# Kernel optimization log

Measured on AMD Instinct MI355X. Metric: run time of the kernel, lower is better.

The kernel has to match this reference:

```python
import jax, jax.numpy as jnp
import numpy as np

H = 256      # hidden_dim
NH = 8       # num_heads
D = H // NH  # per-head dim
NEG = -(2.0**32) + 1.0
EPS = 1e-5


def setup_inputs() -> dict:
    key = jax.random.key(0)
    ks = jax.random.split(key, 12)
    N, Tq, Tk = 2, 2048, 2048
    s = 1.0 / np.sqrt(H)
    return {
        "Q": jax.random.normal(ks[0], (N, Tq, H), jnp.float32),
        "K": jax.random.normal(ks[1], (N, Tk, H), jnp.float32),
        "V": jax.random.normal(ks[2], (N, Tk, H), jnp.float32),
        "Wq": jax.random.normal(ks[3], (H, H), jnp.float32) * s,
        "bq": jnp.zeros((H,), jnp.float32),
        "Wk": jax.random.normal(ks[4], (H, H), jnp.float32) * s,
        "bk": jnp.zeros((H,), jnp.float32),
        "Wv": jax.random.normal(ks[5], (H, H), jnp.float32) * s,
        "bv": jnp.zeros((H,), jnp.float32),
        "gamma": jnp.ones((H,), jnp.float32),
        "beta": jnp.zeros((H,), jnp.float32),
    }


def _split_heads(x):
    # [N,T,H] -> [h,N,T,D]  (matches torch split(dim=2)+cat(dim=0): head-major)
    N, T, _ = x.shape
    return x.reshape(N, T, NH, D).transpose(2, 0, 1, 3)


def reference(Q, K, V, Wq, bq, Wk, bk, Wv, bv, gamma, beta):
    N, Tq, _ = Q.shape
    Tk = K.shape[1]
    Ql = jax.nn.relu(Q @ Wq + bq)
    Kl = jax.nn.relu(K @ Wk + bk)
    Vl = jax.nn.relu(V @ Wv + bv)
    Qh, Kh, Vh = _split_heads(Ql), _split_heads(Kl), _split_heads(Vl)

    scores = jnp.einsum("hnqd,hnkd->hnqk", Qh, Kh) / jnp.sqrt(jnp.float32(D))
    key_mask = jnp.sign(jnp.abs(K).sum(-1))    # [N,Tk]
    scores = jnp.where(key_mask[None, :, None, :] == 0, NEG, scores)
    attn = jax.nn.softmax(scores / 0.01, axis=-1)
    query_mask = jnp.sign(jnp.abs(Q).sum(-1))  # [N,Tq]
    attn = attn * query_mask[None, :, :, None]  # dropout p=0 -> identity

    ctx = jnp.einsum("hnqk,hnkd->hnqd", attn[..., :-1], Vh[:, :, :-1, :])
    out = ctx.transpose(1, 2, 0, 3).reshape(N, Tq, H)

    mu = out.mean(-1, keepdims=True)
    var = ((out - mu) ** 2).mean(-1, keepdims=True)
    out = (out - mu) / jnp.sqrt(var + EPS) * gamma + beta

    weight = attn.transpose(1, 2, 0, 3).reshape(N, Tq, NH * Tk).mean(-1)
    return out, weight
```

## Files before the change

### kernel.cpp

```cpp
#include <hip/hip_runtime.h>
#include <math.h>

#define H_DIM 256
#define NHEAD 8
#define DHEAD 32
#define NB 2
#define TSEQ 2048
#define LN_EPS 1e-5f

#define QK2_SCALE 25.503486f
#define SPLIT 4
#define TILES_PER (TSEQ / 64 / SPLIT)

typedef _Float16 half8 __attribute__((ext_vector_type(8)));
typedef _Float16 half2t __attribute__((ext_vector_type(2)));
typedef float f32x4 __attribute__((ext_vector_type(4)));

__device__ __forceinline__ f32x4 mfma16(half8 a, half8 b, f32x4 c) {
  return __builtin_amdgcn_mfma_f32_16x16x32_f16(a, b, c, 0, 0, 0);
}
__device__ __forceinline__ float exp2fast(float x) {
  return __builtin_amdgcn_exp2f(x);
}
__device__ __forceinline__ half2t pkrtz(float a, float b) {
  return __builtin_bit_cast(half2t, __builtin_amdgcn_cvt_pkrtz(a, b));
}

__global__ __launch_bounds__(256) void mask_kernel(
    const float* __restrict__ Q, const float* __restrict__ K,
    float* __restrict__ qmask, float* __restrict__ kmask) {
  const int wid = threadIdx.x >> 6, lane = threadIdx.x & 63;
  int row = blockIdx.x * 4 + wid;
  const int total_q = NB * TSEQ;
  const float* src;
  float* dst;
  if (row < total_q) { src = Q + (size_t)row * H_DIM; dst = qmask + row; }
  else               { src = K + (size_t)(row - total_q) * H_DIM; dst = kmask + (row - total_q); }
  float4 v = *(const float4*)(src + lane * 4);
  float s = fabsf(v.x) + fabsf(v.y) + fabsf(v.z) + fabsf(v.w);
  #pragma unroll
  for (int off = 32; off > 0; off >>= 1) s += __shfl_xor(s, off);
  if (lane == 0) *dst = (s != 0.0f) ? 1.0f : 0.0f;
}

__global__ __launch_bounds__(256) void prepack_kernel(
    const float* __restrict__ Wq, const float* __restrict__ Wk, const float* __restrict__ Wv,
    half8* __restrict__ WpkHi, half8* __restrict__ WpkLo) {
  int slot = blockIdx.x * 256 + threadIdx.x;
  int lane = slot & 63;
  int fg = (slot >> 6) & 15;
  int s  = (slot >> 10) & 7;
  int which = slot >> 13;
  const float* W = which == 0 ? Wq : which == 1 ? Wk : Wv;
  int j  = fg * 16 + (lane & 15);
  int kb = s * 32 + (lane >> 4) * 8;
  half8 hi, lo;
  #pragma unroll
  for (int jj = 0; jj < 8; ++jj) {
    float x = W[(size_t)(kb + jj) * H_DIM + j];
    _Float16 h = (_Float16)x;
    hi[jj] = h;
    lo[jj] = (_Float16)(x - (float)h);
  }
  WpkHi[slot] = hi;
  WpkLo[slot] = lo;
}

__global__ __launch_bounds__(256) void proj_kernel(
    const float* __restrict__ Q, const float* __restrict__ K, const float* __restrict__ V,
    const float* __restrict__ bq, const float* __restrict__ bk, const float* __restrict__ bv,
    const half8* __restrict__ WpkHi, const half8* __restrict__ WpkLo,
    float* __restrict__ Qh, float* __restrict__ Kh, float* __restrict__ Vh) {
  const int which = blockIdx.z;
  const float* X    = which == 0 ? Q  : which == 1 ? K  : V;
  const float* bias = which == 0 ? bq : which == 1 ? bk : bv;
  float* dst        = which == 0 ? Qh : which == 1 ? Kh : Vh;

  const int tid = threadIdx.x;
  const int w = tid >> 6, lane = tid & 63;
  const int l15 = lane & 15, quad = lane >> 4;
  const int mbase = blockIdx.y * 64;
  const int nfg   = blockIdx.x * 4;

  half8 ahi[8], alo[8];
  {
    const float* xrow = X + (size_t)(mbase + w * 16 + l15) * H_DIM + quad * 8;
    #pragma unroll
    for (int s = 0; s < 8; ++s) {
      float4 a0 = *(const float4*)(xrow + s * 32);
      float4 a1 = *(const float4*)(xrow + s * 32 + 4);
      float xs[8] = {a0.x, a0.y, a0.z, a0.w, a1.x, a1.y, a1.z, a1.w};
      #pragma unroll
      for (int i = 0; i < 8; ++i) {
        _Float16 h = (_Float16)xs[i];
        ahi[s][i] = h;
        alo[s][i] = (_Float16)(xs[i] - (float)h);
      }
    }
  }

  f32x4 acc[4];
  #pragma unroll
  for (int f = 0; f < 4; ++f) acc[f] = (f32x4){0.f, 0.f, 0.f, 0.f};

  #pragma unroll
  for (int s = 0; s < 8; ++s) {
    const half8* ph = WpkHi + (((size_t)which * 8 + s) * 16 + nfg) * 64 + lane;
    const half8* pl = WpkLo + (((size_t)which * 8 + s) * 16 + nfg) * 64 + lane;
    #pragma unroll
    for (int f = 0; f < 4; ++f) {
      half8 BH = ph[f * 64];
      half8 BL = pl[f * 64];
      acc[f] = mfma16(ahi[s], BH, acc[f]);
      acc[f] = mfma16(ahi[s], BL, acc[f]);
      acc[f] = mfma16(alo[s], BH, acc[f]);
    }
  }

  #pragma unroll
  for (int f = 0; f < 4; ++f) {
    int j = blockIdx.x * 64 + f * 16 + l15;
    float bj = bias[j];
    int hh = j >> 5, dd = j & 31;
    #pragma unroll
    for (int r = 0; r < 4; ++r) {
      int m = mbase + w * 16 + quad * 4 + r;
      int n = m >> 11, t = m & (TSEQ - 1);
      float val = fmaxf(acc[f][r] + bj, 0.0f);
      if (which == 2 && t == TSEQ - 1) val = 0.0f;
      dst[(((size_t)hh * NB + n) * TSEQ + t) * DHEAD + dd] = val;
    }
  }
}

__global__ __launch_bounds__(256) void repack_kernel(
    const float* __restrict__ Qh, const float* __restrict__ Kh, const float* __restrict__ Vh,
    const float* __restrict__ kmask,
    half8* __restrict__ Gqhi, half8* __restrict__ Gqlo,
    half8* __restrict__ Gkhi, half8* __restrict__ Gklo, half8* __restrict__ Gv,
    half8* __restrict__ AmaskF) {
  const int tile = blockIdx.x;
  const int hn   = blockIdx.y;
  const int which = blockIdx.z;
  const int tid = threadIdx.x;
  if (which < 2) {
    const int w = tid >> 6, lane = tid & 63;
    const int f = w, krlo = lane & 15, kdc = lane >> 4;
    const float* src = (which == 0 ? Qh : Kh) +
        ((size_t)hn * TSEQ + tile * 64 + f * 16 + krlo) * DHEAD + kdc * 8;
    float4 a0 = *(const float4*)src;
    float4 a1 = *(const float4*)(src + 4);
    float xs[8] = {a0.x, a0.y, a0.z, a0.w, a1.x, a1.y, a1.z, a1.w};
    const float sc = which == 0 ? QK2_SCALE : 1.0f;
    half8 hi, lo;
    #pragma unroll
    for (int i = 0; i < 8; ++i) {
      float x = xs[i] * sc;
      _Float16 h = (_Float16)x;
      hi[i] = h;
      lo[i] = (_Float16)(x - (float)h);
    }
    size_t di = ((size_t)hn * 32 + tile) * 256 + f * 64 + kdc * 16 + krlo;
    if (which == 0) { Gqhi[di] = hi; Gqlo[di] = lo; }
    else            { Gkhi[di] = hi; Gklo[di] = lo; }
  } else if (which == 2) {
    const int s = tid;
    const int top = s >> 6, mid = (s >> 4) & 3, low = s & 15;
    const int c = top >> 1, hh = top & 1;
    const int vkg = c * 4 + mid, vd = hh * 16 + low;
    const int n = hn & 1;
    const float* src = Vh + ((size_t)hn * TSEQ + tile * 64 + vkg * 8) * DHEAD + vd;
    const float* kmp = kmask + (size_t)n * TSEQ + tile * 64 + vkg * 8;
    half8 v8;
    #pragma unroll
    for (int j = 0; j < 8; ++j) v8[j] = (_Float16)(src[j * DHEAD] * kmp[j]);
    Gv[((size_t)hn * 32 + tile) * 256 + s] = v8;
  } else {
    if (hn >= NB || tid >= 128) return;
    const int n = hn;
    const int c = tid >> 6, lane = tid & 63;
    const int quad = lane >> 4, l15 = lane & 15;
    half8 am;
    #pragma unroll
    for (int j = 0; j < 8; ++j)
      am[j] = (l15 == 0) ? (_Float16)kmask[(size_t)n * TSEQ + tile * 64 + c * 32 + quad * 8 + j]
                         : (_Float16)0.0f;
    AmaskF[(((size_t)n * 32 + tile) * 2 + c) * 64 + lane] = am;
  }
}

__global__ __launch_bounds__(256) void attn_kernel(
    const half8* __restrict__ Gqhi, const half8* __restrict__ Gqlo,
    const half8* __restrict__ Gkhi, const half8* __restrict__ Gklo,
    const half8* __restrict__ Gv, const half8* __restrict__ AmaskF,
    float* __restrict__ Op, float* __restrict__ Mp, float* __restrict__ Lp) {
  __shared__ __align__(16) half8 Vf[2][256];
  __shared__ __align__(16) _Float16 Pbuf[4][16][72];

  const int tid = threadIdx.x;
  const int w = tid >> 6, lane = tid & 63;
  const int l15 = lane & 15, quad = lane >> 4;

  const int b = blockIdx.x;
  const int g    = ((b & 7) << 1) | ((b >> 3) & 1);
  const int qt   = (b >> 4) & 31;
  const int sblk = b >> 9;
  const int n = g & 1;

  const size_t fbase = (size_t)g * 32 * 256;
  const int tile0 = sblk * TILES_PER;

  half8 qhi = Gqhi[fbase + (size_t)qt * 256 + w * 64 + lane];
  half8 qlo = Gqlo[fbase + (size_t)qt * 256 + w * 64 + lane];

  float m_q = -1.0e30f;
  f32x4 O0, O1, Ol;
  O0 = (f32x4){0.f, 0.f, 0.f, 0.f};
  O1 = (f32x4){0.f, 0.f, 0.f, 0.f};
  Ol = (f32x4){0.f, 0.f, 0.f, 0.f};

  const half8* kh  = Gkhi + fbase + (size_t)tile0 * 256 + lane;
  const half8* kl  = Gklo + fbase + (size_t)tile0 * 256 + lane;
  const half8* gv  = Gv   + fbase + (size_t)tile0 * 256 + tid;
  const half8* amp = AmaskF + (((size_t)n * 32 + tile0) * 2) * 64 + lane;

  half8 KH[4], KL[4];
  #pragma unroll
  for (int f = 0; f < 4; ++f) { KH[f] = kh[f * 64]; KL[f] = kl[f * 64]; }
  Vf[0][tid] = gv[0];

  #pragma unroll
  for (int tt = 0; tt < TILES_PER; ++tt) {
    half8 KHn[4], KLn[4], vnext;
    if (tt < TILES_PER - 1) {
      #pragma unroll
      for (int f = 0; f < 4; ++f) { KHn[f] = kh[256 + f * 64]; KLn[f] = kl[256 + f * 64]; }
      vnext = gv[256];
    }
    half8 am0 = amp[0];
    half8 am1 = amp[64];

    __syncthreads();
    if (tt < TILES_PER - 1)
      Vf[(tt + 1) & 1][tid] = vnext;

    f32x4 S[4];
    #pragma unroll
    for (int f = 0; f < 4; ++f) {
      f32x4 a = (f32x4){0.f, 0.f, 0.f, 0.f};
      a = mfma16(KL[f], qhi, a);
      a = mfma16(KH[f], qlo, a);
      a = mfma16(KH[f], qhi, a);
      S[f] = a;
    }

    float t0 = fmaxf(fmaxf(S[0][0], S[0][1]), fmaxf(S[0][2], S[0][3]));
    float t1 = fmaxf(fmaxf(S[1][0], S[1][1]), fmaxf(S[1][2], S[1][3]));
    float t2 = fmaxf(fmaxf(S[2][0], S[2][1]), fmaxf(S[2][2], S[2][3]));
    float t3 = fmaxf(fmaxf(S[3][0], S[3][1]), fmaxf(S[3][2], S[3][3]));
    float mx = fmaxf(fmaxf(t0, t1), fmaxf(t2, t3));
    mx = fmaxf(mx, __shfl_xor(mx, 16));
    mx = fmaxf(mx, __shfl_xor(mx, 32));

    float mnew = fmaxf(m_q, mx);
    float alpha = exp2fast(m_q - mnew);
    m_q = mnew;

    #pragma unroll
    for (int f = 0; f < 4; ++f) {
      float p0 = exp2fast(S[f][0] - m_q);
      float p1 = exp2fast(S[f][1] - m_q);
      float p2 = exp2fast(S[f][2] - m_q);
      float p3 = exp2fast(S[f][3] - m_q);
      half2t a01 = pkrtz(p0, p1);
      half2t a23 = pkrtz(p2, p3);
      *(half2t*)&Pbuf[w][l15][f * 16 + quad * 4]     = a01;
      *(half2t*)&Pbuf[w][l15][f * 16 + quad * 4 + 2] = a23;
    }
    #pragma unroll
    for (int r = 0; r < 4; ++r) { O0[r] *= alpha; O1[r] *= alpha; }
    Ol[0] *= alpha;
    asm volatile("s_waitcnt lgkmcnt(0)" ::: "memory");

    const half8* vbuf = (const half8*)Vf[tt & 1];
    #pragma unroll
    for (int c = 0; c < 2; ++c) {
      half8 pb = *(const half8*)&Pbuf[w][l15][c * 32 + quad * 8];
      O0 = mfma16(vbuf[(c * 2 + 0) * 64 + lane], pb, O0);
      O1 = mfma16(vbuf[(c * 2 + 1) * 64 + lane], pb, O1);
      Ol = mfma16(c == 0 ? am0 : am1, pb, Ol);
    }

    #pragma unroll
    for (int f = 0; f < 4; ++f) { KH[f] = KHn[f]; KL[f] = KLn[f]; }
    kh += 256; kl += 256; gv += 256; amp += 128;
  }

  {
    int q = qt * 64 + w * 16 + l15;
    size_t idx = ((size_t)(sblk * 16 + g) * TSEQ + q) * DHEAD;
    *(f32x4*)&Op[idx + quad * 4]      = O0;
    *(f32x4*)&Op[idx + 16 + quad * 4] = O1;
    if (quad == 0) {
      Mp[(size_t)(sblk * 16 + g) * TSEQ + q] = m_q;
      Lp[(size_t)(sblk * 16 + g) * TSEQ + q] = Ol[0];
    }
  }
}

__global__ __launch_bounds__(256) void ln_kernel(
    const float* __restrict__ Op, const float* __restrict__ Mp, const float* __restrict__ Lp,
    const float* __restrict__ gamma, const float* __restrict__ beta,
    const float* __restrict__ qmask,
    float* __restrict__ out, float* __restrict__ wout) {
  const int wid = threadIdx.x >> 6, lane = threadIdx.x & 63;
  const int row = blockIdx.x * 4 + wid;
  const int n = row >> 11, q = row & (TSEQ - 1);
  const int hh = lane >> 3;
  const int hn = hh * NB + n;
  const int dbase = (lane & 7) * 4;

  float4 P[SPLIT];
  float m[SPLIT], l[SPLIT];
  #pragma unroll
  for (int i = 0; i < SPLIT; ++i) {
    size_t si = (size_t)(i * 16 + hn) * TSEQ + q;
    P[i] = *(const float4*)(Op + si * DHEAD + dbase);
    m[i] = Mp[si];
    l[i] = Lp[si];
  }
  float mm = fmaxf(fmaxf(m[0], m[1]), fmaxf(m[2], m[3]));
  float denom = 0.f;
  float a[SPLIT];
  #pragma unroll
  for (int i = 0; i < SPLIT; ++i) { a[i] = exp2fast(m[i] - mm); denom += l[i] * a[i]; }
  float qm = qmask[row];
  float inv = qm / denom;

  float4 x = make_float4(0.f, 0.f, 0.f, 0.f);
  #pragma unroll
  for (int i = 0; i < SPLIT; ++i) {
    x.x += P[i].x * a[i]; x.y += P[i].y * a[i];
    x.z += P[i].z * a[i]; x.w += P[i].w * a[i];
  }
  x.x *= inv; x.y *= inv; x.z *= inv; x.w *= inv;

  float s = x.x + x.y + x.z + x.w;
  #pragma unroll
  for (int off = 32; off > 0; off >>= 1) s += __shfl_xor(s, off);
  float mu = s * (1.0f / H_DIM);
  float dx0 = x.x - mu, dx1 = x.y - mu, dx2 = x.z - mu, dx3 = x.w - mu;
  float sq = dx0 * dx0 + dx1 * dx1 + dx2 * dx2 + dx3 * dx3;
  #pragma unroll
  for (int off = 32; off > 0; off >>= 1) sq += __shfl_xor(sq, off);
  float rstd = rsqrtf(sq * (1.0f / H_DIM) + LN_EPS);
  float4 g = *(const float4*)(gamma + lane * 4);
  float4 bb = *(const float4*)(beta + lane * 4);
  float4 y;
  y.x = dx0 * rstd * g.x + bb.x;
  y.y = dx1 * rstd * g.y + bb.y;
  y.z = dx2 * rstd * g.z + bb.z;
  y.w = dx3 * rstd * g.w + bb.w;
  *(float4*)(out + (size_t)row * H_DIM + lane * 4) = y;
  if (lane == 0) wout[row] = qm * (1.0f / TSEQ);
}

extern "C" void kernel_launch(void* const* d_in, const int* in_sizes, int n_in,
                              void* d_out, int out_size, void* d_ws, size_t ws_size,
                              hipStream_t stream) {
  const float* Q  = (const float*)d_in[0];
  const float* K  = (const float*)d_in[1];
  const float* V  = (const float*)d_in[2];
  const float* Wq = (const float*)d_in[3];
  const float* bq = (const float*)d_in[4];
  const float* Wk = (const float*)d_in[5];
  const float* bk = (const float*)d_in[6];
  const float* Wv = (const float*)d_in[7];
  const float* bv = (const float*)d_in[8];
  const float* gamma = (const float*)d_in[9];
  const float* beta  = (const float*)d_in[10];

  float* ws = (float*)d_ws;
  const size_t perHN = (size_t)16 * TSEQ * DHEAD;
  float* Qh = ws;
  float* Kh = Qh + perHN;
  float* Vh = Kh + perHN;
  float* Opart = ws;
  float* tail = ws + 4 * perHN;
  const size_t NFRAG = (size_t)16 * 32 * 256;
  half8* Gqhi = (half8*)tail;
  half8* Gqlo = Gqhi + NFRAG;
  half8* Gkhi = Gqlo + NFRAG;
  half8* Gklo = Gkhi + NFRAG;
  half8* Gv   = Gklo + NFRAG;
  float* Mp = (float*)(Gv + NFRAG);
  float* Lp = Mp + SPLIT * 16 * TSEQ;
  float* qmask = Lp + SPLIT * 16 * TSEQ;
  float* kmask = qmask + NB * TSEQ;
  half8* WpkHi = (half8*)(kmask + NB * TSEQ);
  half8* WpkLo = WpkHi + 24576;
  half8* AmaskF = WpkLo + 24576;

  float* out  = (float*)d_out;
  float* wout = out + (size_t)NB * TSEQ * H_DIM;

  hipLaunchKernelGGL(mask_kernel, dim3(2 * NB * TSEQ / 4), dim3(256), 0, stream,
                     Q, K, qmask, kmask);
  hipLaunchKernelGGL(prepack_kernel, dim3(96), dim3(256), 0, stream,
                     Wq, Wk, Wv, WpkHi, WpkLo);
  hipLaunchKernelGGL(proj_kernel, dim3(H_DIM / 64, NB * TSEQ / 64, 3), dim3(256), 0, stream,
                     Q, K, V, bq, bk, bv, WpkHi, WpkLo, Qh, Kh, Vh);
  hipLaunchKernelGGL(repack_kernel, dim3(32, 16, 4), dim3(256), 0, stream,
                     Qh, Kh, Vh, kmask, Gqhi, Gqlo, Gkhi, Gklo, Gv, AmaskF);
  hipLaunchKernelGGL(attn_kernel, dim3(16 * 32 * SPLIT), dim3(256), 0, stream,
                     Gqhi, Gqlo, Gkhi, Gklo, Gv, AmaskF, Opart, Mp, Lp);
  hipLaunchKernelGGL(ln_kernel, dim3(NB * TSEQ / 4), dim3(256), 0, stream,
                     Opart, Mp, Lp, gamma, beta, qmask, out, wout);
}
```

Before: 143.3 us.

## Fuse repack into projection via LDS transpose and store attention partials as fp16

```diff
diff --git a/kernel.cpp b/kernel.cpp
--- a/kernel.cpp
+++ b/kernel.cpp
@@ -13,6 +13,7 @@
 #define TILES_PER (TSEQ / 64 / SPLIT)
 
 typedef _Float16 half8 __attribute__((ext_vector_type(8)));
+typedef _Float16 half4t __attribute__((ext_vector_type(4)));
 typedef _Float16 half2t __attribute__((ext_vector_type(2)));
 typedef float f32x4 __attribute__((ext_vector_type(4)));
 
@@ -45,7 +46,24 @@
 
 __global__ __launch_bounds__(256) void prepack_kernel(
     const float* __restrict__ Wq, const float* __restrict__ Wk, const float* __restrict__ Wv,
-    half8* __restrict__ WpkHi, half8* __restrict__ WpkLo) {
+    const float* __restrict__ kmask,
+    half8* __restrict__ WpkHi, half8* __restrict__ WpkLo, half8* __restrict__ AmaskF) {
+  if (blockIdx.x >= 96) {
+    int slot2 = (blockIdx.x - 96) * 256 + threadIdx.x;
+    int n = slot2 >> 12;
+    int rem = slot2 & 4095;
+    int tile = rem >> 7;
+    int c = (rem >> 6) & 1;
+    int lane = rem & 63;
+    int quad = lane >> 4, l15 = lane & 15;
+    half8 am;
+    #pragma unroll
+    for (int j = 0; j < 8; ++j)
+      am[j] = (l15 == 0) ? (_Float16)kmask[(size_t)n * TSEQ + tile * 64 + c * 32 + quad * 8 + j]
+                         : (_Float16)0.0f;
+    AmaskF[(((size_t)n * 32 + tile) * 2 + c) * 64 + lane] = am;
+    return;
+  }
   int slot = blockIdx.x * 256 + threadIdx.x;
   int lane = slot & 63;
   int fg = (slot >> 6) & 15;
@@ -70,17 +88,22 @@
     const float* __restrict__ Q, const float* __restrict__ K, const float* __restrict__ V,
     const float* __restrict__ bq, const float* __restrict__ bk, const float* __restrict__ bv,
     const half8* __restrict__ WpkHi, const half8* __restrict__ WpkLo,
-    float* __restrict__ Qh, float* __restrict__ Kh, float* __restrict__ Vh) {
+    const float* __restrict__ kmask,
+    half8* __restrict__ Gqhi, half8* __restrict__ Gqlo,
+    half8* __restrict__ Gkhi, half8* __restrict__ Gklo, half8* __restrict__ Gv) {
   const int which = blockIdx.z;
   const float* X    = which == 0 ? Q  : which == 1 ? K  : V;
   const float* bias = which == 0 ? bq : which == 1 ? bk : bv;
-  float* dst        = which == 0 ? Qh : which == 1 ? Kh : Vh;
+
+  __shared__ __align__(16) float T[64 * 68];
 
   const int tid = threadIdx.x;
   const int w = tid >> 6, lane = tid & 63;
   const int l15 = lane & 15, quad = lane >> 4;
   const int mbase = blockIdx.y * 64;
   const int nfg   = blockIdx.x * 4;
+  const int nn   = mbase >> 11;
+  const int tile = blockIdx.y & 31;
 
   half8 ahi[8], alo[8];
   {
@@ -119,73 +142,59 @@
 
   #pragma unroll
   for (int f = 0; f < 4; ++f) {
-    int j = blockIdx.x * 64 + f * 16 + l15;
-    float bj = bias[j];
-    int hh = j >> 5, dd = j & 31;
+    float bj = bias[blockIdx.x * 64 + f * 16 + l15];
     #pragma unroll
     for (int r = 0; r < 4; ++r) {
-      int m = mbase + w * 16 + quad * 4 + r;
-      int n = m >> 11, t = m & (TSEQ - 1);
+      int row = w * 16 + quad * 4 + r;
       float val = fmaxf(acc[f][r] + bj, 0.0f);
-      if (which == 2 && t == TSEQ - 1) val = 0.0f;
-      dst[(((size_t)hh * NB + n) * TSEQ + t) * DHEAD + dd] = val;
-    }
-  }
-}
-
-__global__ __launch_bounds__(256) void repack_kernel(
-    const float* __restrict__ Qh, const float* __restrict__ Kh, const float* __restrict__ Vh,
-    const float* __restrict__ kmask,
-    half8* __restrict__ Gqhi, half8* __restrict__ Gqlo,
-    half8* __restrict__ Gkhi, half8* __restrict__ Gklo, half8* __restrict__ Gv,
-    half8* __restrict__ AmaskF) {
-  const int tile = blockIdx.x;
-  const int hn   = blockIdx.y;
-  const int which = blockIdx.z;
-  const int tid = threadIdx.x;
+      if (which == 2 && ((mbase + row) & (TSEQ - 1)) == TSEQ - 1) val = 0.0f;
+      T[row * 68 + f * 16 + l15] = val;
+    }
+  }
+  __syncthreads();
+
   if (which < 2) {
-    const int w = tid >> 6, lane = tid & 63;
-    const int f = w, krlo = lane & 15, kdc = lane >> 4;
-    const float* src = (which == 0 ? Qh : Kh) +
-        ((size_t)hn * TSEQ + tile * 64 + f * 16 + krlo) * DHEAD + kdc * 8;
-    float4 a0 = *(const float4*)src;
-    float4 a1 = *(const float4*)(src + 4);
-    float xs[8] = {a0.x, a0.y, a0.z, a0.w, a1.x, a1.y, a1.z, a1.w};
-    const float sc = which == 0 ? QK2_SCALE : 1.0f;
-    half8 hi, lo;
-    #pragma unroll
-    for (int i = 0; i < 8; ++i) {
-      float x = xs[i] * sc;
-      _Float16 h = (_Float16)x;
-      hi[i] = h;
-      lo[i] = (_Float16)(x - (float)h);
-    }
-    size_t di = ((size_t)hn * 32 + tile) * 256 + f * 64 + kdc * 16 + krlo;
-    if (which == 0) { Gqhi[di] = hi; Gqlo[di] = lo; }
-    else            { Gkhi[di] = hi; Gklo[di] = lo; }
-  } else if (which == 2) {
-    const int s = tid;
-    const int top = s >> 6, mid = (s >> 4) & 3, low = s & 15;
+    const int fq = tid >> 6, lp = tid & 63;
+    const int kdc = lp >> 4, krlo = lp & 15;
+    const int row = fq * 16 + krlo;
+    const float sc = (which == 0) ? QK2_SCALE : 1.0f;
+    #pragma unroll
+    for (int hs = 0; hs < 2; ++hs) {
+      const float* p = &T[row * 68 + hs * 32 + kdc * 8];
+      float4 a0 = *(const float4*)p;
+      float4 a1 = *(const float4*)(p + 4);
+      float xs[8] = {a0.x, a0.y, a0.z, a0.w, a1.x, a1.y, a1.z, a1.w};
+      half8 hi, lo;
+      #pragma unroll
+      for (int i = 0; i < 8; ++i) {
+        float x = xs[i] * sc;
+        _Float16 h = (_Float16)x;
+        hi[i] = h;
+        lo[i] = (_Float16)(x - (float)h);
+      }
+      int hn = (blockIdx.x * 2 + hs) * NB + nn;
+      size_t di = ((size_t)hn * 32 + tile) * 256 + tid;
+      if (which == 0) { Gqhi[di] = hi; Gqlo[di] = lo; }
+      else            { Gkhi[di] = hi; Gklo[di] = lo; }
+    }
+  } else {
+    const int top = tid >> 6, mid = (tid >> 4) & 3, low = tid & 15;
     const int c = top >> 1, hh = top & 1;
-    const int vkg = c * 4 + mid, vd = hh * 16 + low;
-    const int n = hn & 1;
-    const float* src = Vh + ((size_t)hn * TSEQ + tile * 64 + vkg * 8) * DHEAD + vd;
-    const float* kmp = kmask + (size_t)n * TSEQ + tile * 64 + vkg * 8;
-    half8 v8;
-    #pragma unroll
-    for (int j = 0; j < 8; ++j) v8[j] = (_Float16)(src[j * DHEAD] * kmp[j]);
-    Gv[((size_t)hn * 32 + tile) * 256 + s] = v8;
-  } else {
-    if (hn >= NB || tid >= 128) return;
-    const int n = hn;
-    const int c = tid >> 6, lane = tid & 63;
-    const int quad = lane >> 4, l15 = lane & 15;
-    half8 am;
+    const int trow0 = (c * 4 + mid) * 8;
+    float km[8];
     #pragma unroll
     for (int j = 0; j < 8; ++j)
-      am[j] = (l15 == 0) ? (_Float16)kmask[(size_t)n * TSEQ + tile * 64 + c * 32 + quad * 8 + j]
-                         : (_Float16)0.0f;
-    AmaskF[(((size_t)n * 32 + tile) * 2 + c) * 64 + lane] = am;
+      km[j] = kmask[(size_t)nn * TSEQ + tile * 64 + trow0 + j];
+    #pragma unroll
+    for (int hs = 0; hs < 2; ++hs) {
+      const int col = hs * 32 + hh * 16 + low;
+      half8 v8;
+      #pragma unroll
+      for (int j = 0; j < 8; ++j)
+        v8[j] = (_Float16)(T[(trow0 + j) * 68 + col] * km[j]);
+      int hn = (blockIdx.x * 2 + hs) * NB + nn;
+      Gv[((size_t)hn * 32 + tile) * 256 + tid] = v8;
+    }
   }
 }
 
@@ -193,7 +202,7 @@
     const half8* __restrict__ Gqhi, const half8* __restrict__ Gqlo,
     const half8* __restrict__ Gkhi, const half8* __restrict__ Gklo,
     const half8* __restrict__ Gv, const half8* __restrict__ AmaskF,
-    float* __restrict__ Op, float* __restrict__ Mp, float* __restrict__ Lp) {
+    _Float16* __restrict__ Opf, float* __restrict__ Mp, float* __restrict__ Lp) {
   __shared__ __align__(16) half8 Vf[2][256];
   __shared__ __align__(16) _Float16 Pbuf[4][16][72];
 
@@ -299,8 +308,10 @@
   {
     int q = qt * 64 + w * 16 + l15;
     size_t idx = ((size_t)(sblk * 16 + g) * TSEQ + q) * DHEAD;
-    *(f32x4*)&Op[idx + quad * 4]      = O0;
-    *(f32x4*)&Op[idx + 16 + quad * 4] = O1;
+    half4t o0 = {(_Float16)O0[0], (_Float16)O0[1], (_Float16)O0[2], (_Float16)O0[3]};
+    half4t o1 = {(_Float16)O1[0], (_Float16)O1[1], (_Float16)O1[2], (_Float16)O1[3]};
+    *(half4t*)&Opf[idx + quad * 4]      = o0;
+    *(half4t*)&Opf[idx + 16 + quad * 4] = o1;
     if (quad == 0) {
       Mp[(size_t)(sblk * 16 + g) * TSEQ + q] = m_q;
       Lp[(size_t)(sblk * 16 + g) * TSEQ + q] = Ol[0];
@@ -309,7 +320,7 @@
 }
 
 __global__ __launch_bounds__(256) void ln_kernel(
-    const float* __restrict__ Op, const float* __restrict__ Mp, const float* __restrict__ Lp,
+    const _Float16* __restrict__ Opf, const float* __restrict__ Mp, const float* __restrict__ Lp,
     const float* __restrict__ gamma, const float* __restrict__ beta,
     const float* __restrict__ qmask,
     float* __restrict__ out, float* __restrict__ wout) {
@@ -320,12 +331,12 @@
   const int hn = hh * NB + n;
   const int dbase = (lane & 7) * 4;
 
-  float4 P[SPLIT];
   float m[SPLIT], l[SPLIT];
+  half4t P[SPLIT];
   #pragma unroll
   for (int i = 0; i < SPLIT; ++i) {
     size_t si = (size_t)(i * 16 + hn) * TSEQ + q;
-    P[i] = *(const float4*)(Op + si * DHEAD + dbase);
+    P[i] = *(const half4t*)&Opf[si * DHEAD + dbase];
     m[i] = Mp[si];
     l[i] = Lp[si];
   }
@@ -340,8 +351,8 @@
   float4 x = make_float4(0.f, 0.f, 0.f, 0.f);
   #pragma unroll
   for (int i = 0; i < SPLIT; ++i) {
-    x.x += P[i].x * a[i]; x.y += P[i].y * a[i];
-    x.z += P[i].z * a[i]; x.w += P[i].w * a[i];
+    x.x += (float)P[i][0] * a[i]; x.y += (float)P[i][1] * a[i];
+    x.z += (float)P[i][2] * a[i]; x.w += (float)P[i][3] * a[i];
   }
   x.x *= inv; x.y *= inv; x.z *= inv; x.w *= inv;
 
@@ -380,15 +391,10 @@
   const float* gamma = (const float*)d_in[9];
   const float* beta  = (const float*)d_in[10];
 
-  float* ws = (float*)d_ws;
-  const size_t perHN = (size_t)16 * TSEQ * DHEAD;
-  float* Qh = ws;
-  float* Kh = Qh + perHN;
-  float* Vh = Kh + perHN;
-  float* Opart = ws;
-  float* tail = ws + 4 * perHN;
+  char* ws = (char*)d_ws;
   const size_t NFRAG = (size_t)16 * 32 * 256;
-  half8* Gqhi = (half8*)tail;
+  _Float16* Opf = (_Float16*)ws;
+  half8* Gqhi = (half8*)(ws + (size_t)SPLIT * 16 * TSEQ * DHEAD * 2);
   half8* Gqlo = Gqhi + NFRAG;
   half8* Gkhi = Gqlo + NFRAG;
   half8* Gklo = Gkhi + NFRAG;
@@ -406,14 +412,13 @@
 
   hipLaunchKernelGGL(mask_kernel, dim3(2 * NB * TSEQ / 4), dim3(256), 0, stream,
                      Q, K, qmask, kmask);
-  hipLaunchKernelGGL(prepack_kernel, dim3(96), dim3(256), 0, stream,
-                     Wq, Wk, Wv, WpkHi, WpkLo);
+  hipLaunchKernelGGL(prepack_kernel, dim3(128), dim3(256), 0, stream,
+                     Wq, Wk, Wv, kmask, WpkHi, WpkLo, AmaskF);
   hipLaunchKernelGGL(proj_kernel, dim3(H_DIM / 64, NB * TSEQ / 64, 3), dim3(256), 0, stream,
-                     Q, K, V, bq, bk, bv, WpkHi, WpkLo, Qh, Kh, Vh);
-  hipLaunchKernelGGL(repack_kernel, dim3(32, 16, 4), dim3(256), 0, stream,
-                     Qh, Kh, Vh, kmask, Gqhi, Gqlo, Gkhi, Gklo, Gv, AmaskF);
+                     Q, K, V, bq, bk, bv, WpkHi, WpkLo, kmask,
+                     Gqhi, Gqlo, Gkhi, Gklo, Gv);
   hipLaunchKernelGGL(attn_kernel, dim3(16 * 32 * SPLIT), dim3(256), 0, stream,
-                     Gqhi, Gqlo, Gkhi, Gklo, Gv, AmaskF, Opart, Mp, Lp);
+                     Gqhi, Gqlo, Gkhi, Gklo, Gv, AmaskF, Opf, Mp, Lp);
   hipLaunchKernelGGL(ln_kernel, dim3(NB * TSEQ / 4), dim3(256), 0, stream,
-                     Opart, Mp, Lp, gamma, beta, qmask, out, wout);
-}
+                     Opf, Mp, Lp, gamma, beta, qmask, out, wout);
+}
```

Measured after the change: 131.8 us. 8.0% less time.
